# Optimization experiments

Hardware: AMD Instinct MI355X
Metric: run time of the kernel (lower is better)

The kernel has to match this reference:

```python
import jax, jax.numpy as jnp
import numpy as np

H = 16  # num attention heads
D = 1024  # hidden size
F = 4096  # intermediate size
LN_EPS = 1e-5


def _glorot(key, shape):
    fan_in, fan_out = shape[0], shape[1]
    lim = np.sqrt(6.0 / (fan_in + fan_out))
    return jax.random.uniform(key, shape, jnp.float32, -lim, lim)


def setup_inputs() -> dict:
    key = jax.random.key(0)
    ks = jax.random.split(key, 16)
    inp = {
        'input_tensor': jax.random.normal(ks[0], (4, 1024, D), jnp.float32),
        'ctx_tensor': jax.random.normal(ks[1], (4, 2048, D), jnp.float32),
        'ctx_attn_mask': jnp.zeros((4, 1, 1, 2048), jnp.float32),
        # cross-attention QKV
        'cq_w': _glorot(ks[2], (D, D)), 'cq_b': jnp.zeros((D,)),
        'ck_w': _glorot(ks[3], (D, D)), 'ck_b': jnp.zeros((D,)),
        'cv_w': _glorot(ks[4], (D, D)), 'cv_b': jnp.zeros((D,)),
        # cross output (dense + LN)
        'co_w': _glorot(ks[5], (D, D)), 'co_b': jnp.zeros((D,)),
        'co_g': jnp.ones((D,)), 'co_be': jnp.zeros((D,)),
        # self-attention QKV
        'sq_w': _glorot(ks[6], (D, D)), 'sq_b': jnp.zeros((D,)),
        'sk_w': _glorot(ks[7], (D, D)), 'sk_b': jnp.zeros((D,)),
        'sv_w': _glorot(ks[8], (D, D)), 'sv_b': jnp.zeros((D,)),
        # self-attention output
        'so_w': _glorot(ks[9], (D, D)), 'so_b': jnp.zeros((D,)),
        'so_g': jnp.ones((D,)), 'so_be': jnp.zeros((D,)),
        # FFN intermediate + output
        'fi_w': _glorot(ks[10], (D, F)), 'fi_b': jnp.zeros((F,)),
        'fo_w': _glorot(ks[11], (F, D)), 'fo_b': jnp.zeros((D,)),
        'fo_g': jnp.ones((D,)), 'fo_be': jnp.zeros((D,)),
    }
    return inp


def _split_heads(x):
    b, l, _ = x.shape
    return x.reshape(b, l, H, D // H)


def _mha(x, ctx, mask, qw, qb, kw, kb, vw, vb):
    # manual QK^T/sqrt(d) -> +mask -> softmax -> V (dropout=0 / eval)
    q = _split_heads(x @ qw + qb)       # [b, lq, h, d]
    k = _split_heads(ctx @ kw + kb)     # [b, lk, h, d]
    v = _split_heads(ctx @ vw + vb)
    scores = jnp.einsum('bqhd,bkhd->bhqk', q, k) / np.sqrt(D // H).astype(np.float32)
    if mask is not None:
        scores = scores + mask
    probs = jax.nn.softmax(scores, axis=-1)
    out = jnp.einsum('bhqk,bkhd->bqhd', probs, v)
    return out.reshape(x.shape[0], x.shape[1], D)


def _self_output(h, residual, w, b, g, be):
    h = h @ w + b
    h = h + residual
    mu = jnp.mean(h, axis=-1, keepdims=True)
    var = jnp.mean(jnp.square(h - mu), axis=-1, keepdims=True)
    return (h - mu) * jax.lax.rsqrt(var + LN_EPS) * g + be


def reference(input_tensor, ctx_tensor, ctx_attn_mask,
              cq_w, cq_b, ck_w, ck_b, cv_w, cv_b, co_w, co_b, co_g, co_be,
              sq_w, sq_b, sk_w, sk_b, sv_w, sv_b, so_w, so_b, so_g, so_be,
              fi_w, fi_b, fo_w, fo_b, fo_g, fo_be):
    # CrossLayer.forward
    ca = _mha(input_tensor, ctx_tensor, ctx_attn_mask, cq_w, cq_b, ck_w, ck_b, cv_w, cv_b)
    x = _self_output(ca, input_tensor, co_w, co_b, co_g, co_be)
    sa = _mha(x, x, None, sq_w, sq_b, sk_w, sk_b, sv_w, sv_b)
    x = _self_output(sa, x, so_w, so_b, so_g, so_be)
    inter = jax.nn.gelu(x @ fi_w + fi_b, approximate=False)
    x = _self_output(inter, x, fo_w, fo_b, fo_g, fo_be)
    return x
```

## Files before the change

### kernel.cpp

```cpp
#include <hip/hip_runtime.h>
#include <math.h>

typedef unsigned short ushort_t;
typedef __bf16 bf16x8 __attribute__((ext_vector_type(8)));
typedef float f32x4 __attribute__((ext_vector_type(4)));

__device__ __forceinline__ float bf2f(unsigned int u) {
    union { unsigned int i; float f; } v; v.i = u << 16; return v.f;
}
__device__ __forceinline__ ushort_t f2bf(float f) {
    union { float f; unsigned int i; } v; v.f = f;
    unsigned int u = v.i;
    unsigned int r = u + 0x7fffu + ((u >> 16) & 1u);
    return (ushort_t)(r >> 16);
}

__device__ __forceinline__ void gload16(const ushort_t* g, ushort_t* l) {
    __builtin_amdgcn_global_load_lds(
        (__attribute__((address_space(1))) void*)g,
        (__attribute__((address_space(3))) void*)l, 16, 0, 0);
}

__global__ void __launch_bounds__(256) cvt_bf16_kernel(
    const float* __restrict__ in, ushort_t* __restrict__ out, int n8)
{
    int i = blockIdx.x * 256 + threadIdx.x;
    if (i >= n8) return;
    size_t off = (size_t)i * 8;
    float4 a = *(const float4*)(in + off);
    float4 b = *(const float4*)(in + off + 4);
    ushort_t o[8] = {f2bf(a.x), f2bf(a.y), f2bf(a.z), f2bf(a.w),
                     f2bf(b.x), f2bf(b.y), f2bf(b.z), f2bf(b.w)};
    *(uint4*)(out + off) = *(const uint4*)o;
}

__global__ void __launch_bounds__(256) wconv_kernel(
    const float* __restrict__ W, ushort_t* __restrict__ Wt, int K, int N)
{
    __shared__ float tile[32][33];
    const int t = threadIdx.x;
    const int k0 = blockIdx.x * 32, n0 = blockIdx.y * 32;
    const int r = t >> 3, c4 = (t & 7) * 4;
    float4 d = *(const float4*)(&W[(size_t)(k0 + r) * N + n0 + c4]);
    tile[r][c4 + 0] = d.x; tile[r][c4 + 1] = d.y;
    tile[r][c4 + 2] = d.z; tile[r][c4 + 3] = d.w;
    __syncthreads();
    ushort_t o[4] = { f2bf(tile[c4 + 0][r]), f2bf(tile[c4 + 1][r]),
                      f2bf(tile[c4 + 2][r]), f2bf(tile[c4 + 3][r]) };
    *(uint2*)(&Wt[(size_t)(n0 + r) * K + k0 + c4]) = *(const uint2*)o;
}

#define BM 128
#define BK 32

template <int MODE, int BNT>
__global__ void __launch_bounds__(256) gemm_bt_kernel(
    const ushort_t* __restrict__ A,
    const ushort_t* __restrict__ B0, const ushort_t* __restrict__ B1,
    const ushort_t* __restrict__ B2,
    const float* __restrict__ bias0, const float* __restrict__ bias1,
    const float* __restrict__ bias2,
    ushort_t* __restrict__ C0, ushort_t* __restrict__ C1,
    ushort_t* __restrict__ C2,
    int M, int N, int K)
{
    __shared__ __align__(16) ushort_t As[2][BM * BK];
    __shared__ __align__(16) ushort_t Bs[2][BNT * BK];

    constexpr int NJ = BNT / 32;
    constexpr int WN = BNT / 2;

    const int z = blockIdx.z;
    const ushort_t* Bt = (z == 0) ? B0 : ((z == 1) ? B1 : B2);
    const float* bias = (z == 0) ? bias0 : ((z == 1) ? bias1 : bias2);
    ushort_t* Cout = (z == 0) ? C0 : ((z == 1) ? C1 : C2);

    const int tid = threadIdx.x;
    const int m0 = blockIdx.y * BM, n0 = blockIdx.x * BNT;
    const int wave = tid >> 6, lane = tid & 63;
    const int wm = wave >> 1, wn = wave & 1;
    const int lr = lane & 15;
    const int lk = (lane >> 4) * 8;

    const ushort_t* Ab = A + (size_t)m0 * K;
    const ushort_t* Bb = Bt + (size_t)n0 * K;
    const int srow = tid >> 2;
    const int sc8 = (tid & 3) * 8;

    f32x4 acc[4][NJ];
#pragma unroll
    for (int i = 0; i < 4; i++)
#pragma unroll
        for (int j = 0; j < NJ; j++) acc[i][j] = (f32x4){0.f, 0.f, 0.f, 0.f};

    const int nt = K / BK;

    {
        const size_t ga = (size_t)srow * K + sc8;
        gload16(Ab + ga,                  &As[0][tid * 8]);
        gload16(Ab + ga + (size_t)64 * K, &As[0][2048 + tid * 8]);
        gload16(Bb + ga,                  &Bs[0][tid * 8]);
        if (BNT == 128)
            gload16(Bb + ga + (size_t)64 * K, &Bs[0][2048 + tid * 8]);
    }
    asm volatile("s_waitcnt vmcnt(0)" ::: "memory");
    __syncthreads();

    int cur = 0;
    for (int t = 0; t < nt; ++t) {
        if (t + 1 < nt) {
            const size_t ga = (size_t)srow * K + (size_t)(t + 1) * BK + sc8;
            gload16(Ab + ga,                  &As[cur ^ 1][tid * 8]);
            gload16(Ab + ga + (size_t)64 * K, &As[cur ^ 1][2048 + tid * 8]);
            gload16(Bb + ga,                  &Bs[cur ^ 1][tid * 8]);
            if (BNT == 128)
                gload16(Bb + ga + (size_t)64 * K, &Bs[cur ^ 1][2048 + tid * 8]);
        }
        bf16x8 af[4], bfr[NJ];
#pragma unroll
        for (int i = 0; i < 4; i++)
            af[i] = *(const bf16x8*)(&As[cur][(wm * 64 + i * 16 + lr) * BK + lk]);
#pragma unroll
        for (int j = 0; j < NJ; j++)
            bfr[j] = *(const bf16x8*)(&Bs[cur][(wn * WN + j * 16 + lr) * BK + lk]);
#pragma unroll
        for (int i = 0; i < 4; i++)
#pragma unroll
            for (int j = 0; j < NJ; j++)
                acc[i][j] = __builtin_amdgcn_mfma_f32_16x16x32_bf16(af[i], bfr[j], acc[i][j], 0, 0, 0);
        asm volatile("s_waitcnt vmcnt(0)" ::: "memory");
        __syncthreads();
        cur ^= 1;
    }

    const int rq = (lane >> 4) * 4;
#pragma unroll
    for (int j = 0; j < NJ; j++) {
        const int col = n0 + wn * WN + j * 16 + lr;
        const float bv = bias[col];
#pragma unroll
        for (int i = 0; i < 4; i++) {
#pragma unroll
            for (int r = 0; r < 4; r++) {
                const int row = m0 + wm * 64 + i * 16 + rq + r;
                float v = acc[i][j][r] + bv;
                if (MODE == 2) {
                    v = 0.5f * v * (1.0f + erff(v * 0.70710678118654752f));
                }
                Cout[(size_t)row * N + col] = f2bf(v);
            }
        }
    }
}

__global__ void __launch_bounds__(256) mfma_attn_kernel(
    const ushort_t* __restrict__ Q, const ushort_t* __restrict__ Kt,
    const ushort_t* __restrict__ Vt, const float* __restrict__ mask,
    ushort_t* __restrict__ O, int Lq, int Lk, float scale)
{
    __shared__ __align__(16) ushort_t qs[64][72];
    __shared__ __align__(16) ushort_t ks[64][72];
    __shared__ __align__(16) ushort_t vsT[64][72];
    __shared__ __align__(16) ushort_t ps[4][16][72];

    const int tid = threadIdx.x;
    const int wave = tid >> 6, lane = tid & 63;
    const int quad = lane >> 4, lc = lane & 15;

    const int id = blockIdx.x + (int)gridDim.x * blockIdx.y;
    const int bh = (id & 7) * 8 + ((id >> 3) >> 4);
    const int qt = (id >> 3) & 15;
    const int b = bh >> 4, h = bh & 15;
    const int q0 = qt * 64;
    const size_t qbase = ((size_t)b * Lq) * 1024 + h * 64;
    const size_t kbase = ((size_t)b * Lk) * 1024 + h * 64;
    const float* maskb = mask ? (mask + (size_t)b * Lk) : nullptr;

#pragma unroll
    for (int r = 0; r < 2; r++) {
        int v = r * 256 + tid;
        int row = v >> 3, c8 = (v & 7) * 8;
        *(uint4*)(&qs[row][c8]) = *(const uint4*)(&Q[qbase + (size_t)(q0 + row) * 1024 + c8]);
    }
    __syncthreads();

    bf16x8 qa0 = *(const bf16x8*)(&qs[wave * 16 + lc][quad * 8]);
    bf16x8 qa1 = *(const bf16x8*)(&qs[wave * 16 + lc][32 + quad * 8]);

    f32x4 o[4];
#pragma unroll
    for (int d = 0; d < 4; d++) o[d] = (f32x4){0.f, 0.f, 0.f, 0.f};
    float m_i[4], l_i[4];
#pragma unroll
    for (int r = 0; r < 4; r++) { m_i[r] = -1e30f; l_i[r] = 0.f; }

    const int sr = tid >> 2;
    const int d0c = (tid & 3) * 16;
    const int vswz = (tid & 3) << 3;
    const int vcol = sr ^ vswz;

    const int nt = Lk >> 6;
    size_t gk = kbase + (size_t)sr * 1024 + d0c;

    uint4 kA = *(const uint4*)(Kt + gk);
    uint4 kB = *(const uint4*)(Kt + gk + 8);
    uint4 vA = *(const uint4*)(Vt + gk);
    uint4 vB = *(const uint4*)(Vt + gk + 8);

    for (int t = 0; t < nt; ++t) {
        const int kt = t << 6;
        __syncthreads();
        *(uint4*)(&ks[sr][d0c])     = kA;
        *(uint4*)(&ks[sr][d0c + 8]) = kB;
        {
            const ushort_t* vp = (const ushort_t*)&vA;
            const ushort_t* wp = (const ushort_t*)&vB;
#pragma unroll
            for (int i = 0; i < 8; i++) vsT[d0c + i][vcol]     = vp[i];
#pragma unroll
            for (int i = 0; i < 8; i++) vsT[d0c + 8 + i][vcol] = wp[i];
        }
        if (t + 1 < nt) {
            gk += 64 * 1024;
            kA = *(const uint4*)(Kt + gk);
            kB = *(const uint4*)(Kt + gk + 8);
            vA = *(const uint4*)(Vt + gk);
            vB = *(const uint4*)(Vt + gk + 8);
        }
        __syncthreads();

        float mk[4];
#pragma unroll
        for (int g = 0; g < 4; g++)
            mk[g] = maskb ? maskb[kt + g * 16 + lc] : 0.f;

        f32x4 s[4];
        __builtin_amdgcn_s_setprio(1);
#pragma unroll
        for (int g = 0; g < 4; g++) {
            bf16x8 k0 = *(const bf16x8*)(&ks[g * 16 + lc][quad * 8]);
            bf16x8 k1 = *(const bf16x8*)(&ks[g * 16 + lc][32 + quad * 8]);
            f32x4 z = (f32x4){0.f, 0.f, 0.f, 0.f};
            z = __builtin_amdgcn_mfma_f32_16x16x32_bf16(qa0, k0, z, 0, 0, 0);
            z = __builtin_amdgcn_mfma_f32_16x16x32_bf16(qa1, k1, z, 0, 0, 0);
            s[g] = z;
        }
        __builtin_amdgcn_s_setprio(0);

        float alpha[4];
#pragma unroll
        for (int r = 0; r < 4; r++) {
            float v0 = s[0][r] * scale + mk[0];
            float v1 = s[1][r] * scale + mk[1];
            float v2 = s[2][r] * scale + mk[2];
            float v3 = s[3][r] * scale + mk[3];
            float mx = fmaxf(fmaxf(v0, v1), fmaxf(v2, v3));
#pragma unroll
            for (int off = 1; off < 16; off <<= 1) mx = fmaxf(mx, __shfl_xor(mx, off, 64));
            float mnew = fmaxf(m_i[r], mx);
            alpha[r] = __expf(m_i[r] - mnew);
            m_i[r] = mnew;
            float p0 = __expf(v0 - mnew);
            float p1 = __expf(v1 - mnew);
            float p2 = __expf(v2 - mnew);
            float p3 = __expf(v3 - mnew);
            ps[wave][quad * 4 + r][lc]      = f2bf(p0);
            ps[wave][quad * 4 + r][16 + lc] = f2bf(p1);
            ps[wave][quad * 4 + r][32 + lc] = f2bf(p2);
            ps[wave][quad * 4 + r][48 + lc] = f2bf(p3);
            float psum = (p0 + p1) + (p2 + p3);
#pragma unroll
            for (int off = 1; off < 16; off <<= 1) psum += __shfl_xor(psum, off, 64);
            l_i[r] = l_i[r] * alpha[r] + psum;
        }
#pragma unroll
        for (int d = 0; d < 4; d++)
#pragma unroll
            for (int r = 0; r < 4; r++) o[d][r] *= alpha[r];

        __builtin_amdgcn_s_setprio(1);
#pragma unroll
        for (int kk = 0; kk < 2; kk++) {
            bf16x8 pa = *(const bf16x8*)(&ps[wave][lc][kk * 32 + quad * 8]);
#pragma unroll
            for (int d = 0; d < 4; d++) {
                int dr = d * 16 + lc;
                bf16x8 vb = *(const bf16x8*)(&vsT[dr][(kk * 32 + quad * 8) ^ (d << 3)]);
                o[d] = __builtin_amdgcn_mfma_f32_16x16x32_bf16(pa, vb, o[d], 0, 0, 0);
            }
        }
        __builtin_amdgcn_s_setprio(0);
    }

#pragma unroll
    for (int d = 0; d < 4; d++) {
#pragma unroll
        for (int r = 0; r < 4; r++) {
            float val = o[d][r] / l_i[r];
            O[qbase + (size_t)(q0 + wave * 16 + quad * 4 + r) * 1024 + d * 16 + lc] = f2bf(val);
        }
    }
}

template <bool RES_F32, bool OUT_F32>
__global__ void __launch_bounds__(256) ln_kernel(
    const ushort_t* __restrict__ Hbuf, const void* __restrict__ Res,
    const float* __restrict__ gamma, const float* __restrict__ beta,
    void* __restrict__ Out)
{
    const int row = blockIdx.x;
    const int tid = threadIdx.x;
    const size_t base = (size_t)row * 1024 + tid * 4;

    uint2 hh = *(const uint2*)(Hbuf + base);
    float v[4];
    v[0] = bf2f(hh.x & 0xffffu);
    v[1] = bf2f(hh.x >> 16);
    v[2] = bf2f(hh.y & 0xffffu);
    v[3] = bf2f(hh.y >> 16);
    if (RES_F32) {
        float4 rv = *(const float4*)((const float*)Res + base);
        v[0] += rv.x; v[1] += rv.y; v[2] += rv.z; v[3] += rv.w;
    } else {
        uint2 rr = *(const uint2*)((const ushort_t*)Res + base);
        v[0] += bf2f(rr.x & 0xffffu);
        v[1] += bf2f(rr.x >> 16);
        v[2] += bf2f(rr.y & 0xffffu);
        v[3] += bf2f(rr.y >> 16);
    }

    float s = v[0] + v[1] + v[2] + v[3];
    float s2 = v[0]*v[0] + v[1]*v[1] + v[2]*v[2] + v[3]*v[3];
#pragma unroll
    for (int o = 1; o < 64; o <<= 1) {
        s += __shfl_xor(s, o, 64);
        s2 += __shfl_xor(s2, o, 64);
    }
    __shared__ float red[8];
    const int wv = tid >> 6, ln_ = tid & 63;
    if (ln_ == 0) { red[wv] = s; red[wv + 4] = s2; }
    __syncthreads();
    s = red[0] + red[1] + red[2] + red[3];
    s2 = red[4] + red[5] + red[6] + red[7];
    const float mu = s * (1.0f / 1024.0f);
    const float var = s2 * (1.0f / 1024.0f) - mu * mu;
    const float rstd = rsqrtf(var + 1e-5f);

    float4 gv = *(const float4*)(&gamma[tid * 4]);
    float4 bv = *(const float4*)(&beta[tid * 4]);
    float o0 = (v[0] - mu) * rstd * gv.x + bv.x;
    float o1 = (v[1] - mu) * rstd * gv.y + bv.y;
    float o2 = (v[2] - mu) * rstd * gv.z + bv.z;
    float o3 = (v[3] - mu) * rstd * gv.w + bv.w;

    if (OUT_F32) {
        float4 of = {o0, o1, o2, o3};
        *(float4*)((float*)Out + base) = of;
    } else {
        ushort_t ob[4] = {f2bf(o0), f2bf(o1), f2bf(o2), f2bf(o3)};
        *(uint2*)((ushort_t*)Out + base) = *(uint2*)ob;
    }
}

extern "C" void kernel_launch(void* const* d_in, const int* in_sizes, int n_in,
                              void* d_out, int out_size, void* d_ws, size_t ws_size,
                              hipStream_t stream)
{
    const float* input = (const float*)d_in[0];
    const float* ctx   = (const float*)d_in[1];
    const float* mask  = (const float*)d_in[2];
    const float* cq_w = (const float*)d_in[3],  *cq_b = (const float*)d_in[4];
    const float* ck_w = (const float*)d_in[5],  *ck_b = (const float*)d_in[6];
    const float* cv_w = (const float*)d_in[7],  *cv_b = (const float*)d_in[8];
    const float* co_w = (const float*)d_in[9],  *co_b = (const float*)d_in[10];
    const float* co_g = (const float*)d_in[11], *co_be = (const float*)d_in[12];
    const float* sq_w = (const float*)d_in[13], *sq_b = (const float*)d_in[14];
    const float* sk_w = (const float*)d_in[15], *sk_b = (const float*)d_in[16];
    const float* sv_w = (const float*)d_in[17], *sv_b = (const float*)d_in[18];
    const float* so_w = (const float*)d_in[19], *so_b = (const float*)d_in[20];
    const float* so_g = (const float*)d_in[21], *so_be = (const float*)d_in[22];
    const float* fi_w = (const float*)d_in[23], *fi_b = (const float*)d_in[24];
    const float* fo_w = (const float*)d_in[25], *fo_b = (const float*)d_in[26];
    const float* fo_g = (const float*)d_in[27], *fo_be = (const float*)d_in[28];

    char* p = (char*)d_ws;
    const size_t MB = 1024 * 1024;
    ushort_t* Bq   = (ushort_t*)(p + 0 * MB);
    ushort_t* Bk   = (ushort_t*)(p + 8 * MB);
    ushort_t* Bv   = (ushort_t*)(p + 24 * MB);
    ushort_t* Ba   = (ushort_t*)(p + 40 * MB);
    ushort_t* Bh   = (ushort_t*)(p + 48 * MB);
    ushort_t* Bx1  = (ushort_t*)(p + 56 * MB);
    ushort_t* Bx2  = (ushort_t*)(p + 64 * MB);
    ushort_t* Bi   = Bk;
    ushort_t* Xctx = Ba;
    ushort_t* Xin  = Bx2;
    ushort_t* WtA  = (ushort_t*)(p + 56 * MB);
    ushort_t* WtB  = (ushort_t*)(p + 58 * MB);
    ushort_t* WtC  = (ushort_t*)(p + 60 * MB);
    ushort_t* WtD  = (ushort_t*)(p + 64 * MB);
    ushort_t* WtE  = (ushort_t*)(p + 66 * MB);
    ushort_t* WtF  = (ushort_t*)(p + 68 * MB);
    ushort_t* WtG  = (ushort_t*)(p + 0 * MB);

    const float scale = 0.125f;
    dim3 blk(256);

    cvt_bf16_kernel<<<2048, blk, 0, stream>>>(input, Xin, 524288);
    cvt_bf16_kernel<<<4096, blk, 0, stream>>>(ctx, Xctx, 1048576);

    wconv_kernel<<<dim3(32, 32), blk, 0, stream>>>(cq_w, WtA, 1024, 1024);
    wconv_kernel<<<dim3(32, 32), blk, 0, stream>>>(ck_w, WtB, 1024, 1024);
    wconv_kernel<<<dim3(32, 32), blk, 0, stream>>>(cv_w, WtC, 1024, 1024);
    gemm_bt_kernel<0, 64><<<dim3(16, 32, 1), blk, 0, stream>>>(
        Xin, WtA, WtA, WtA, cq_b, cq_b, cq_b, Bq, Bq, Bq, 4096, 1024, 1024);
    gemm_bt_kernel<0, 64><<<dim3(16, 64, 2), blk, 0, stream>>>(
        Xctx, WtB, WtC, WtC, ck_b, cv_b, cv_b, Bk, Bv, Bv, 8192, 1024, 1024);
    mfma_attn_kernel<<<dim3(16, 64), blk, 0, stream>>>(Bq, Bk, Bv, mask, Ba, 1024, 2048, scale);
    wconv_kernel<<<dim3(32, 32), blk, 0, stream>>>(co_w, WtA, 1024, 1024);
    gemm_bt_kernel<0, 64><<<dim3(16, 32, 1), blk, 0, stream>>>(
        Ba, WtA, WtA, WtA, co_b, co_b, co_b, Bh, Bh, Bh, 4096, 1024, 1024);
    ln_kernel<true, false><<<dim3(4096), blk, 0, stream>>>(Bh, input, co_g, co_be, Bx1);

    wconv_kernel<<<dim3(32, 32), blk, 0, stream>>>(sq_w, WtD, 1024, 1024);
    wconv_kernel<<<dim3(32, 32), blk, 0, stream>>>(sk_w, WtE, 1024, 1024);
    wconv_kernel<<<dim3(32, 32), blk, 0, stream>>>(sv_w, WtF, 1024, 1024);
    gemm_bt_kernel<0, 64><<<dim3(16, 32, 3), blk, 0, stream>>>(
        Bx1, WtD, WtE, WtF, sq_b, sk_b, sv_b, Bq, Bk, Bv, 4096, 1024, 1024);
    mfma_attn_kernel<<<dim3(16, 64), blk, 0, stream>>>(Bq, Bk, Bv, nullptr, Ba, 1024, 1024, scale);
    wconv_kernel<<<dim3(32, 32), blk, 0, stream>>>(so_w, WtD, 1024, 1024);
    gemm_bt_kernel<0, 64><<<dim3(16, 32, 1), blk, 0, stream>>>(
        Ba, WtD, WtD, WtD, so_b, so_b, so_b, Bh, Bh, Bh, 4096, 1024, 1024);
    ln_kernel<false, false><<<dim3(4096), blk, 0, stream>>>(Bh, Bx1, so_g, so_be, Bx2);

    wconv_kernel<<<dim3(32, 128), blk, 0, stream>>>(fi_w, WtG, 1024, 4096);
    gemm_bt_kernel<2, 128><<<dim3(32, 32, 1), blk, 0, stream>>>(
        Bx2, WtG, WtG, WtG, fi_b, fi_b, fi_b, Bi, Bi, Bi, 4096, 4096, 1024);
    wconv_kernel<<<dim3(128, 32), blk, 0, stream>>>(fo_w, WtG, 4096, 1024);
    gemm_bt_kernel<0, 64><<<dim3(16, 32, 1), blk, 0, stream>>>(
        Bi, WtG, WtG, WtG, fo_b, fo_b, fo_b, Bh, Bh, Bh, 4096, 1024, 4096);
    ln_kernel<false, true><<<dim3(4096), blk, 0, stream>>>(Bh, Bx2, fo_g, fo_be, (float*)d_out);
}
```

Before: 718.8 us.

## Triple-buffer GEMM loads and use DPP row rotates in attention softmax

The GEMM moves from double to triple buffering in LDS. Loads are issued two tiles ahead and a partial vmcnt wait keeps the newest tile's loads in flight while the current tile is computed. The attention kernel replaces the shuffle-based 16-lane max and sum reductions with DPP row-rotate moves, and uses the hardware bf16 conversion for probabilities and outputs. The extra LDS buffer raises shared memory per block, which may lower occupancy, and the vmcnt counts are hard-coded to the number of loads per stage.

```diff
diff --git a/kernel.cpp b/kernel.cpp
--- a/kernel.cpp
+++ b/kernel.cpp
@@ -13,6 +13,16 @@
     unsigned int u = v.i;
     unsigned int r = u + 0x7fffu + ((u >> 16) & 1u);
     return (ushort_t)(r >> 16);
+}
+__device__ __forceinline__ ushort_t f2bf_hw(float f) {
+    union { __bf16 h; ushort_t u; } v; v.h = (__bf16)f; return v.u;
+}
+
+template <int N>
+__device__ __forceinline__ float ror16f(float x) {
+    union { float f; int i; } u; u.f = x;
+    u.i = __builtin_amdgcn_mov_dpp(u.i, 0x120 + N, 0xF, 0xF, true);
+    return u.f;
 }
 
 __device__ __forceinline__ void gload16(const ushort_t* g, ushort_t* l) {
@@ -64,8 +74,8 @@
     ushort_t* __restrict__ C2,
     int M, int N, int K)
 {
-    __shared__ __align__(16) ushort_t As[2][BM * BK];
-    __shared__ __align__(16) ushort_t Bs[2][BNT * BK];
+    __shared__ __align__(16) ushort_t As[3][BM * BK];
+    __shared__ __align__(16) ushort_t Bs[3][BNT * BK];
 
     constexpr int NJ = BNT / 32;
     constexpr int WN = BNT / 2;
@@ -95,27 +105,32 @@
 
     const int nt = K / BK;
 
-    {
-        const size_t ga = (size_t)srow * K + sc8;
-        gload16(Ab + ga,                  &As[0][tid * 8]);
-        gload16(Ab + ga + (size_t)64 * K, &As[0][2048 + tid * 8]);
-        gload16(Bb + ga,                  &Bs[0][tid * 8]);
+    auto stage = [&](int buf, int t) {
+        const size_t ga = (size_t)srow * K + (size_t)t * BK + sc8;
+        gload16(Ab + ga,                  &As[buf][tid * 8]);
+        gload16(Ab + ga + (size_t)64 * K, &As[buf][2048 + tid * 8]);
+        gload16(Bb + ga,                  &Bs[buf][tid * 8]);
         if (BNT == 128)
-            gload16(Bb + ga + (size_t)64 * K, &Bs[0][2048 + tid * 8]);
-    }
-    asm volatile("s_waitcnt vmcnt(0)" ::: "memory");
-    __syncthreads();
+            gload16(Bb + ga + (size_t)64 * K, &Bs[buf][2048 + tid * 8]);
+    };
+
+    stage(0, 0);
+    stage(1, 1);
 
     int cur = 0;
     for (int t = 0; t < nt; ++t) {
-        if (t + 1 < nt) {
-            const size_t ga = (size_t)srow * K + (size_t)(t + 1) * BK + sc8;
-            gload16(Ab + ga,                  &As[cur ^ 1][tid * 8]);
-            gload16(Ab + ga + (size_t)64 * K, &As[cur ^ 1][2048 + tid * 8]);
-            gload16(Bb + ga,                  &Bs[cur ^ 1][tid * 8]);
+        if (t + 2 < nt) {
+            int nxt = cur + 2; if (nxt >= 3) nxt -= 3;
+            stage(nxt, t + 2);
             if (BNT == 128)
-                gload16(Bb + ga + (size_t)64 * K, &Bs[cur ^ 1][2048 + tid * 8]);
-        }
+                asm volatile("s_waitcnt vmcnt(8)" ::: "memory");
+            else
+                asm volatile("s_waitcnt vmcnt(6)" ::: "memory");
+        } else {
+            asm volatile("s_waitcnt vmcnt(0)" ::: "memory");
+        }
+        __syncthreads();
+
         bf16x8 af[4], bfr[NJ];
 #pragma unroll
         for (int i = 0; i < 4; i++)
@@ -128,9 +143,8 @@
 #pragma unroll
             for (int j = 0; j < NJ; j++)
                 acc[i][j] = __builtin_amdgcn_mfma_f32_16x16x32_bf16(af[i], bfr[j], acc[i][j], 0, 0, 0);
-        asm volatile("s_waitcnt vmcnt(0)" ::: "memory");
         __syncthreads();
-        cur ^= 1;
+        cur = (cur == 2) ? 0 : cur + 1;
     }
 
     const int rq = (lane >> 4) * 4;
@@ -240,10 +254,10 @@
         for (int g = 0; g < 4; g++) {
             bf16x8 k0 = *(const bf16x8*)(&ks[g * 16 + lc][quad * 8]);
             bf16x8 k1 = *(const bf16x8*)(&ks[g * 16 + lc][32 + quad * 8]);
-            f32x4 z = (f32x4){0.f, 0.f, 0.f, 0.f};
-            z = __builtin_amdgcn_mfma_f32_16x16x32_bf16(qa0, k0, z, 0, 0, 0);
-            z = __builtin_amdgcn_mfma_f32_16x16x32_bf16(qa1, k1, z, 0, 0, 0);
-            s[g] = z;
+            f32x4 zz = (f32x4){0.f, 0.f, 0.f, 0.f};
+            zz = __builtin_amdgcn_mfma_f32_16x16x32_bf16(qa0, k0, zz, 0, 0, 0);
+            zz = __builtin_amdgcn_mfma_f32_16x16x32_bf16(qa1, k1, zz, 0, 0, 0);
+            s[g] = zz;
         }
         __builtin_amdgcn_s_setprio(0);
 
@@ -255,8 +269,10 @@
             float v2 = s[2][r] * scale + mk[2];
             float v3 = s[3][r] * scale + mk[3];
             float mx = fmaxf(fmaxf(v0, v1), fmaxf(v2, v3));
-#pragma unroll
-            for (int off = 1; off < 16; off <<= 1) mx = fmaxf(mx, __shfl_xor(mx, off, 64));
+            mx = fmaxf(mx, ror16f<1>(mx));
+            mx = fmaxf(mx, ror16f<2>(mx));
+            mx = fmaxf(mx, ror16f<4>(mx));
+            mx = fmaxf(mx, ror16f<8>(mx));
             float mnew = fmaxf(m_i[r], mx);
             alpha[r] = __expf(m_i[r] - mnew);
             m_i[r] = mnew;
@@ -264,13 +280,15 @@
             float p1 = __expf(v1 - mnew);
             float p2 = __expf(v2 - mnew);
             float p3 = __expf(v3 - mnew);
-            ps[wave][quad * 4 + r][lc]      = f2bf(p0);
-            ps[wave][quad * 4 + r][16 + lc] = f2bf(p1);
-            ps[wave][quad * 4 + r][32 + lc] = f2bf(p2);
-            ps[wave][quad * 4 + r][48 + lc] = f2bf(p3);
+            ps[wave][quad * 4 + r][lc]      = f2bf_hw(p0);
+            ps[wave][quad * 4 + r][16 + lc] = f2bf_hw(p1);
+            ps[wave][quad * 4 + r][32 + lc] = f2bf_hw(p2);
+            ps[wave][quad * 4 + r][48 + lc] = f2bf_hw(p3);
             float psum = (p0 + p1) + (p2 + p3);
-#pragma unroll
-            for (int off = 1; off < 16; off <<= 1) psum += __shfl_xor(psum, off, 64);
+            psum += ror16f<1>(psum);
+            psum += ror16f<2>(psum);
+            psum += ror16f<4>(psum);
+            psum += ror16f<8>(psum);
             l_i[r] = l_i[r] * alpha[r] + psum;
         }
 #pragma unroll
@@ -297,7 +315,7 @@
 #pragma unroll
         for (int r = 0; r < 4; r++) {
             float val = o[d][r] / l_i[r];
-            O[qbase + (size_t)(q0 + wave * 16 + quad * 4 + r) * 1024 + d * 16 + lc] = f2bf(val);
+            O[qbase + (size_t)(q0 + wave * 16 + quad * 4 + r) * 1024 + d * 16 + lc] = f2bf_hw(val);
         }
     }
 }
```

Result: faster. 691.6 us (-3.8%).
